# Optimization experiments

Hardware: AMD Instinct MI355X
Metric: run time of the kernel (lower is better)

The kernel has to match this reference:

```python
import jax, jax.numpy as jnp
import numpy as np

SIGMA = 1.0
DELTA = 1.0
TOPK = 10
TOPK_HALF = int(np.around(TOPK / 2))  # 5
EPS = 1e-12


def _cdist(a, b):
    # Euclidean distance matrix, grad-safe sqrt at zero (matches torch.cdist values).
    d2 = (jnp.sum(a * a, axis=1)[:, None]
          + jnp.sum(b * b, axis=1)[None, :]
          - 2.0 * (a @ b.T))
    d2 = jnp.maximum(d2, 0.0)
    pos = d2 > 0.0
    return jnp.where(pos, jnp.sqrt(jnp.where(pos, d2, 1.0)), 0.0)


def _consistency_weights(t_emb):
    # Everything here is under torch.no_grad() in the original.
    N = t_emb.shape[0]
    T_dist = _cdist(t_emb, t_emb)
    W_P = jnp.exp(-(T_dist ** 2) / SIGMA)
    _, idx = jax.lax.top_k(W_P, TOPK)                      # [N, TOPK]
    rows = jnp.arange(N)[:, None]
    W_NN = jnp.zeros_like(W_P).at[rows, idx].set(1.0)      # scatter_ ones
    V = (((W_NN + W_NN.T) / 2) == 1.0).astype(W_P.dtype)   # mutual kNN (symmetric)
    # Vectorized form of the per-row python loop:
    #   W_C_tilda[i, j] = V[i, j] * (sum_k V[i, k] * V[j, k]) / sum_k V[i, k]
    deg = jnp.sum(V, axis=1)                               # >= 1 (self is always a NN)
    overlap = V @ V.T                                      # [N, N] neighbor overlap
    W_C_tilda = V * overlap / deg[:, None]
    topk_half_index = idx[:, :TOPK_HALF]                   # [N, TOPK_HALF]
    W_C_hat = jnp.mean(W_C_tilda[topk_half_index], axis=1) # gather rows, mean -> [N, N]
    W_C = (W_C_hat + W_C_hat.T) / 2
    return (W_P + W_C) / 2


def reference(s_emb, t_emb):
    # disable_mu = 0 -> s_emb NOT normalized; t_emb always normalized.
    t_norm = t_emb / jnp.maximum(
        jnp.linalg.norm(t_emb, axis=1, keepdims=True), EPS)
    N = s_emb.shape[0]
    S_dist = _cdist(s_emb, s_emb)
    S_dist = S_dist / jnp.mean(S_dist, axis=1, keepdims=True)
    W = jax.lax.stop_gradient(_consistency_weights(t_norm))
    off_diag = 1.0 - jnp.eye(N, dtype=W.dtype)
    pos_weight = W * off_diag
    neg_weight = (1.0 - W) * off_diag
    pull = jnp.maximum(S_dist, 0.0) ** 2 * pos_weight
    push = jnp.maximum(DELTA - S_dist, 0.0) ** 2 * neg_weight
    return (jnp.sum(pull) + jnp.sum(push)) / (N * (N - 1))


def setup_inputs() -> dict:
    key = jax.random.key(0)
    k1, k2 = jax.random.split(key)
    N, D = 2048, 1024
    return {
        "s_emb": jax.random.normal(k1, (N, D), dtype=jnp.float32),
        "t_emb": jax.random.normal(k2, (N, D), dtype=jnp.float32),
    }
```

## Files before the change

kernel.cpp:

```cpp
#include <hip/hip_runtime.h>
#include <math.h>

#define N_ 2048
#define D_ 1024
#define TOPK 10
#define TOPK_HALF 5
#define INV_NORM (1.0f / ((float)N_ * (float)(N_ - 1)))

typedef __attribute__((ext_vector_type(8))) short short8;
typedef __attribute__((ext_vector_type(4))) float floatx4;

__device__ __forceinline__ short f2bf(float f) {
  unsigned u = __float_as_uint(f);
  unsigned r = (u + 0x7fffu + ((u >> 16) & 1u)) >> 16;
  return (short)r;
}
__device__ __forceinline__ float bf2f(short b) {
  return __uint_as_float(((unsigned)(unsigned short)b) << 16);
}

__device__ __forceinline__ void gld_lds16(const short* g, short* l) {
  __builtin_amdgcn_global_load_lds(
      (const __attribute__((address_space(1))) unsigned int*)(g),
      (__attribute__((address_space(3))) unsigned int*)(l), 16, 0, 0);
}

__global__ __launch_bounds__(256) void prep_kernel(const float* __restrict__ t,
                                                   const float* __restrict__ s,
                                                   short* __restrict__ tb,
                                                   short* __restrict__ sb,
                                                   float* __restrict__ tt,
                                                   float* __restrict__ ss,
                                                   float* __restrict__ rowsum,
                                                   float* __restrict__ out) {
  int b = blockIdx.x, tid = threadIdx.x;
  __shared__ float red[256];
  if (b == 0) {
    for (int j = tid; j < N_; j += 256) rowsum[j] = 0.f;
    if (tid == 0) out[0] = 0.f;
  }
  if (b < N_) {
    const float* rp = t + (size_t)b * D_;
    short* op = tb + (size_t)b * D_;
    float acc = 0.f;
    for (int k = tid; k < D_; k += 256) { float v = rp[k]; acc += v * v; }
    red[tid] = acc; __syncthreads();
    for (int st = 128; st > 0; st >>= 1) { if (tid < st) red[tid] += red[tid + st]; __syncthreads(); }
    float denom = fmaxf(sqrtf(red[0]), 1e-12f);
    __syncthreads();
    float s2 = 0.f;
    for (int k = tid; k < D_; k += 256) { float v = rp[k] / denom; op[k] = f2bf(v); s2 += v * v; }
    red[tid] = s2; __syncthreads();
    for (int st = 128; st > 0; st >>= 1) { if (tid < st) red[tid] += red[tid + st]; __syncthreads(); }
    if (tid == 0) tt[b] = red[0];
  } else {
    int row = b - N_;
    const float* rp = s + (size_t)row * D_;
    short* op = sb + (size_t)row * D_;
    float acc = 0.f;
    for (int k = tid; k < D_; k += 256) { float v = rp[k]; op[k] = f2bf(v); acc += v * v; }
    red[tid] = acc; __syncthreads();
    for (int st = 128; st > 0; st >>= 1) { if (tid < st) red[tid] += red[tid + st]; __syncthreads(); }
    if (tid == 0) ss[row] = red[0];
  }
}

__global__ __launch_bounds__(256) void gram_mfma_kernel(
    const short* __restrict__ Tb, const short* __restrict__ Sb,
    const float* __restrict__ tt, const float* __restrict__ ss,
    short* __restrict__ WPb, short* __restrict__ Sob,
    float* __restrict__ rowsum) {
  const int mode = blockIdx.z;
  const short* A = mode ? Sb : Tb;
  const float* rn = mode ? ss : tt;
  short* outb = mode ? Sob : WPb;

  __shared__ __align__(16) short As[128 * 64];
  __shared__ __align__(16) short Bs[128 * 64];

  int tid = threadIdx.x;
  int w = tid >> 6, lane = tid & 63;
  int i0 = blockIdx.y * 128, j0 = blockIdx.x * 128;
  int wr = w >> 1, wc = w & 1;
  int quad = lane >> 4, l16 = lane & 15;

  floatx4 acc[4][4] = {};

  int srow = w * 32 + (lane >> 3);
  int scol = (lane & 7) * 8;
  const short* Ag = A + (size_t)(i0 + srow) * D_ + scol;
  const short* Bg = A + (size_t)(j0 + srow) * D_ + scol;
  short* Al = As + srow * 64 + scol;
  short* Bl = Bs + srow * 64 + scol;

  for (int k0 = 0; k0 < D_; k0 += 64) {
    __syncthreads();
#pragma unroll
    for (int q = 0; q < 4; q++) {
      gld_lds16(Ag + k0 + (size_t)q * 8 * D_, Al + q * 8 * 64);
      gld_lds16(Bg + k0 + (size_t)q * 8 * D_, Bl + q * 8 * 64);
    }
    __syncthreads();
#pragma unroll
    for (int ks = 0; ks < 64; ks += 32) {
      short8 af[4], bfr[4];
#pragma unroll
      for (int mt = 0; mt < 4; mt++)
        af[mt] = *(const short8*)&As[(wr * 64 + mt * 16 + l16) * 64 + ks + quad * 8];
#pragma unroll
      for (int nt = 0; nt < 4; nt++)
        bfr[nt] = *(const short8*)&Bs[(wc * 64 + nt * 16 + l16) * 64 + ks + quad * 8];
#pragma unroll
      for (int mt = 0; mt < 4; mt++)
#pragma unroll
        for (int nt = 0; nt < 4; nt++)
          acc[mt][nt] = __builtin_amdgcn_mfma_f32_16x16x32_bf16(af[mt], bfr[nt], acc[mt][nt], 0, 0, 0);
    }
  }

#pragma unroll
  for (int mt = 0; mt < 4; mt++) {
#pragma unroll
    for (int r = 0; r < 4; r++) {
      int i = i0 + wr * 64 + mt * 16 + quad * 4 + r;
      float ri = rn[i];
      float rs = 0.f;
#pragma unroll
      for (int nt = 0; nt < 4; nt++) {
        int j = j0 + wc * 64 + nt * 16 + l16;
        float d2 = fmaxf(ri + rn[j] - 2.f * acc[mt][nt][r], 0.f);
        float o = mode ? sqrtf(d2) : expf(-d2);
        if (i == j) o = mode ? 0.f : 1.f;
        outb[(size_t)i * N_ + j] = f2bf(o);
        rs += o;
      }
      if (mode) {
        rs += __shfl_xor(rs, 1); rs += __shfl_xor(rs, 2);
        rs += __shfl_xor(rs, 4); rs += __shfl_xor(rs, 8);
        if (l16 == 0) atomicAdd(&rowsum[i], rs);
      }
    }
  }
}

__global__ __launch_bounds__(256) void topk_loss_kernel(const short* __restrict__ WPb,
                                                        const short* __restrict__ Sb,
                                                        const float* __restrict__ rowsum,
                                                        int* __restrict__ idx,
                                                        float* __restrict__ out) {
  int row = blockIdx.x, tid = threadIdx.x;
  short8 wp8 = ((const short8*)(WPb + (size_t)row * N_))[tid];
  short8 s8 = ((const short8*)(Sb + (size_t)row * N_))[tid];
  float w[8];
  float rminv = (float)N_ / rowsum[row];
  float local = 0.f;
#pragma unroll
  for (int c = 0; c < 8; c++) {
    w[c] = bf2f(wp8[c]);
    float sv = bf2f(s8[c]) * rminv;
    float d = fmaxf(1.0f - sv, 0.f);
    local += d * d + 0.5f * w[c] * (sv * sv - d * d);
  }
  __shared__ float red[256];
  __shared__ float wv[4];
  __shared__ int wi[4];
  red[tid] = local; __syncthreads();
  for (int st = 128; st > 0; st >>= 1) { if (tid < st) red[tid] += red[tid + st]; __syncthreads(); }
  if (tid == 0) atomicAdd(out, (red[0] - 0.5f) * INV_NORM);

  for (int t = 0; t < TOPK; t++) {
    float bv = -2.f; int bi = 0;
#pragma unroll
    for (int c = 0; c < 8; c++)
      if (w[c] > bv) { bv = w[c]; bi = tid * 8 + c; }
#pragma unroll
    for (int off = 32; off > 0; off >>= 1) {
      float ov = __shfl_down(bv, off);
      int oi = __shfl_down(bi, off);
      if (ov > bv || (ov == bv && oi < bi)) { bv = ov; bi = oi; }
    }
    __syncthreads();
    if ((tid & 63) == 0) { wv[tid >> 6] = bv; wi[tid >> 6] = bi; }
    __syncthreads();
    float b0 = wv[0]; int j0w = wi[0];
#pragma unroll
    for (int u = 1; u < 4; u++)
      if (wv[u] > b0 || (wv[u] == b0 && wi[u] < j0w)) { b0 = wv[u]; j0w = wi[u]; }
    if (tid == 0) idx[row * TOPK + t] = j0w;
    if ((j0w >> 3) == tid) w[j0w & 7] = -1.f;
  }
}

__global__ void mutual_kernel(const int* __restrict__ idx, int* __restrict__ nbr,
                              int* __restrict__ deg) {
  int i = blockIdx.x * blockDim.x + threadIdx.x;
  if (i >= N_) return;
  int cnt = 0;
  for (int k = 0; k < TOPK; k++) {
    int j = idx[i * TOPK + k];
    bool mut = false;
    for (int l = 0; l < TOPK; l++)
      if (idx[j * TOPK + l] == i) mut = true;
    if (mut) nbr[i * TOPK + cnt++] = j;
  }
  deg[i] = cnt;
}

__global__ __launch_bounds__(256) void sparse_wc_kernel(
    const int* __restrict__ idx, const int* __restrict__ nbr,
    const int* __restrict__ deg, const short* __restrict__ Sb,
    const float* __restrict__ rowsum, float* __restrict__ out) {
  int t = blockIdx.x * 256 + threadIdx.x;
  int i = t / (TOPK_HALF * TOPK);
  int r = t % (TOPK_HALF * TOPK);
  int mi = r / TOPK, k = r % TOPK;
  float contrib = 0.f;
  if (i < N_) {
    int m = idx[i * TOPK + mi];
    int dm = deg[m];
    if (k < dm) {
      int col = nbr[m * TOPK + k];
      if (col != i) {
        int dj = deg[col];
        int c = 0;
        for (int a = 0; a < dm; a++) {
          int na = nbr[m * TOPK + a];
          for (int b = 0; b < dj; b++) c += (nbr[col * TOPK + b] == na);
        }
        float v = (float)c / (float)dm * 0.1f;
        float s1 = bf2f(Sb[(size_t)i * N_ + col]) * ((float)N_ / rowsum[i]);
        float d1 = fmaxf(1.f - s1, 0.f);
        float s2 = bf2f(Sb[(size_t)col * N_ + i]) * ((float)N_ / rowsum[col]);
        float d2 = fmaxf(1.f - s2, 0.f);
        contrib = 0.5f * v * ((s1 * s1 - d1 * d1) + (s2 * s2 - d2 * d2));
      }
    }
  }
  __shared__ float red[256];
  red[threadIdx.x] = contrib; __syncthreads();
  for (int st = 128; st > 0; st >>= 1) {
    if (threadIdx.x < st) red[threadIdx.x] += red[threadIdx.x + st];
    __syncthreads();
  }
  if (threadIdx.x == 0) atomicAdd(out, red[0] * INV_NORM);
}

#define SPARSE_BLOCKS ((N_ * TOPK_HALF * TOPK) / 256)

extern "C" void kernel_launch(void* const* d_in, const int* in_sizes, int n_in,
                              void* d_out, int out_size, void* d_ws, size_t ws_size,
                              hipStream_t stream) {
  const float* s_emb = (const float*)d_in[0];
  const float* t_emb = (const float*)d_in[1];
  float* out = (float*)d_out;

  const size_t NN = (size_t)N_ * N_;
  const size_t ND = (size_t)N_ * D_;
  short* t_bf = (short*)d_ws;
  short* s_bf = t_bf + ND;
  short* WPb = s_bf + ND;
  short* Sb = WPb + NN;
  float* tt = (float*)(Sb + NN);
  float* ss = tt + N_;
  float* rowsum = ss + N_;
  int* idx = (int*)(rowsum + N_);
  int* nbr = idx + (size_t)N_ * TOPK;
  int* deg = nbr + (size_t)N_ * TOPK;

  prep_kernel<<<2 * N_, 256, 0, stream>>>(t_emb, s_emb, t_bf, s_bf, tt, ss, rowsum, out);

  dim3 g(N_ / 128, N_ / 128, 2);
  gram_mfma_kernel<<<g, 256, 0, stream>>>(t_bf, s_bf, tt, ss, WPb, Sb, rowsum);

  topk_loss_kernel<<<N_, 256, 0, stream>>>(WPb, Sb, rowsum, idx, out);
  mutual_kernel<<<N_ / 256, 256, 0, stream>>>(idx, nbr, deg);
  sparse_wc_kernel<<<SPARSE_BLOCKS, 256, 0, stream>>>(idx, nbr, deg, Sb, rowsum, out);
}
```

Measured before the change: 172.0 us.

## Double-buffer and swizzle GEMM LDS tiles; use single-wave topk and bitmask mutual kNN

```diff
diff --git a/kernel.cpp b/kernel.cpp
--- a/kernel.cpp
+++ b/kernel.cpp
@@ -24,6 +24,10 @@
       (const __attribute__((address_space(1))) unsigned int*)(g),
       (__attribute__((address_space(3))) unsigned int*)(l), 16, 0, 0);
 }
+
+#define BAR() asm volatile("s_barrier" ::: "memory")
+#define WAIT8_BAR() asm volatile("s_waitcnt vmcnt(8)\ns_barrier" ::: "memory")
+#define WAIT0_BAR() asm volatile("s_waitcnt vmcnt(0)\ns_barrier" ::: "memory")
 
 __global__ __launch_bounds__(256) void prep_kernel(const float* __restrict__ t,
                                                    const float* __restrict__ s,
@@ -75,8 +79,8 @@
   const float* rn = mode ? ss : tt;
   short* outb = mode ? Sob : WPb;
 
-  __shared__ __align__(16) short As[128 * 64];
-  __shared__ __align__(16) short Bs[128 * 64];
+  __shared__ __align__(16) short As[2][128 * 64];
+  __shared__ __align__(16) short Bs[2][128 * 64];
 
   int tid = threadIdx.x;
   int w = tid >> 6, lane = tid & 63;
@@ -87,29 +91,46 @@
   floatx4 acc[4][4] = {};
 
   int srow = w * 32 + (lane >> 3);
-  int scol = (lane & 7) * 8;
-  const short* Ag = A + (size_t)(i0 + srow) * D_ + scol;
-  const short* Bg = A + (size_t)(j0 + srow) * D_ + scol;
-  short* Al = As + srow * 64 + scol;
-  short* Bl = Bs + srow * 64 + scol;
-
-  for (int k0 = 0; k0 < D_; k0 += 64) {
-    __syncthreads();
-#pragma unroll
-    for (int q = 0; q < 4; q++) {
-      gld_lds16(Ag + k0 + (size_t)q * 8 * D_, Al + q * 8 * 64);
-      gld_lds16(Bg + k0 + (size_t)q * 8 * D_, Bl + q * 8 * 64);
-    }
-    __syncthreads();
+  int gchunk = ((lane & 7) ^ (lane >> 3)) * 8;
+  const short* Ag = A + (size_t)(i0 + srow) * D_ + gchunk;
+  const short* Bg = A + (size_t)(j0 + srow) * D_ + gchunk;
+  int sloc = srow * 64 + (lane & 7) * 8;
+
+#define STAGE(buf, k0)                                        \
+  do {                                                        \
+    _Pragma("unroll") for (int q = 0; q < 4; q++) {           \
+      gld_lds16(Ag + (k0) + (size_t)q * 8 * D_, &As[buf][sloc + q * 8 * 64]); \
+      gld_lds16(Bg + (k0) + (size_t)q * 8 * D_, &Bs[buf][sloc + q * 8 * 64]); \
+    }                                                         \
+  } while (0)
+
+  STAGE(0, 0);
+#pragma unroll 2
+  for (int it = 0; it < 16; it++) {
+    int cur = it & 1;
+    if (it) BAR();
+    if (it < 15) {
+      STAGE(!cur, (it + 1) * 64);
+      WAIT8_BAR();
+    } else {
+      WAIT0_BAR();
+    }
+    const short* Ab = As[cur];
+    const short* Bb = Bs[cur];
 #pragma unroll
     for (int ks = 0; ks < 64; ks += 32) {
+      int cb = ks >> 3;
       short8 af[4], bfr[4];
 #pragma unroll
-      for (int mt = 0; mt < 4; mt++)
-        af[mt] = *(const short8*)&As[(wr * 64 + mt * 16 + l16) * 64 + ks + quad * 8];
-#pragma unroll
-      for (int nt = 0; nt < 4; nt++)
-        bfr[nt] = *(const short8*)&Bs[(wc * 64 + nt * 16 + l16) * 64 + ks + quad * 8];
+      for (int mt = 0; mt < 4; mt++) {
+        int r = wr * 64 + mt * 16 + l16;
+        af[mt] = *(const short8*)&Ab[r * 64 + (((cb + quad) ^ (l16 & 7)) << 3)];
+      }
+#pragma unroll
+      for (int nt = 0; nt < 4; nt++) {
+        int r = wc * 64 + nt * 16 + l16;
+        bfr[nt] = *(const short8*)&Bb[r * 64 + (((cb + quad) ^ (l16 & 7)) << 3)];
+      }
 #pragma unroll
       for (int mt = 0; mt < 4; mt++)
 #pragma unroll
@@ -143,89 +164,105 @@
   }
 }
 
-__global__ __launch_bounds__(256) void topk_loss_kernel(const short* __restrict__ WPb,
-                                                        const short* __restrict__ Sb,
-                                                        const float* __restrict__ rowsum,
-                                                        int* __restrict__ idx,
-                                                        float* __restrict__ out) {
-  int row = blockIdx.x, tid = threadIdx.x;
-  short8 wp8 = ((const short8*)(WPb + (size_t)row * N_))[tid];
-  short8 s8 = ((const short8*)(Sb + (size_t)row * N_))[tid];
-  float w[8];
+__global__ __launch_bounds__(64) void topk_loss_kernel(const short* __restrict__ WPb,
+                                                       const short* __restrict__ Sb,
+                                                       const float* __restrict__ rowsum,
+                                                       int* __restrict__ idx,
+                                                       unsigned* __restrict__ mask,
+                                                       float* __restrict__ out) {
+  int row = blockIdx.x, lane = threadIdx.x;
+  const short8* wpr = (const short8*)(WPb + (size_t)row * N_);
+  const short8* sr = (const short8*)(Sb + (size_t)row * N_);
   float rminv = (float)N_ / rowsum[row];
+  float w[32];
   float local = 0.f;
 #pragma unroll
-  for (int c = 0; c < 8; c++) {
-    w[c] = bf2f(wp8[c]);
-    float sv = bf2f(s8[c]) * rminv;
-    float d = fmaxf(1.0f - sv, 0.f);
-    local += d * d + 0.5f * w[c] * (sv * sv - d * d);
-  }
-  __shared__ float red[256];
-  __shared__ float wv[4];
-  __shared__ int wi[4];
-  red[tid] = local; __syncthreads();
-  for (int st = 128; st > 0; st >>= 1) { if (tid < st) red[tid] += red[tid + st]; __syncthreads(); }
-  if (tid == 0) atomicAdd(out, (red[0] - 0.5f) * INV_NORM);
-
+  for (int c4 = 0; c4 < 4; c4++) {
+    short8 wp8 = wpr[lane * 4 + c4];
+    short8 s8 = sr[lane * 4 + c4];
+#pragma unroll
+    for (int e = 0; e < 8; e++) {
+      float wv = bf2f(wp8[e]);
+      w[c4 * 8 + e] = wv;
+      float sv = bf2f(s8[e]) * rminv;
+      float d = fmaxf(1.f - sv, 0.f);
+      local += d * d + 0.5f * wv * (sv * sv - d * d);
+    }
+  }
+#pragma unroll
+  for (int off = 32; off > 0; off >>= 1) local += __shfl_down(local, off);
+  if (lane == 0) {
+    atomicAdd(out, (local - 0.5f) * INV_NORM);
+    mask[row] = 0u;
+  }
+  int base = lane * 32;
+  int sel[TOPK];
   for (int t = 0; t < TOPK; t++) {
     float bv = -2.f; int bi = 0;
 #pragma unroll
-    for (int c = 0; c < 8; c++)
-      if (w[c] > bv) { bv = w[c]; bi = tid * 8 + c; }
+    for (int c = 0; c < 32; c++)
+      if (w[c] > bv) { bv = w[c]; bi = base + c; }
 #pragma unroll
     for (int off = 32; off > 0; off >>= 1) {
       float ov = __shfl_down(bv, off);
       int oi = __shfl_down(bi, off);
       if (ov > bv || (ov == bv && oi < bi)) { bv = ov; bi = oi; }
     }
-    __syncthreads();
-    if ((tid & 63) == 0) { wv[tid >> 6] = bv; wi[tid >> 6] = bi; }
-    __syncthreads();
-    float b0 = wv[0]; int j0w = wi[0];
-#pragma unroll
-    for (int u = 1; u < 4; u++)
-      if (wv[u] > b0 || (wv[u] == b0 && wi[u] < j0w)) { b0 = wv[u]; j0w = wi[u]; }
-    if (tid == 0) idx[row * TOPK + t] = j0w;
-    if ((j0w >> 3) == tid) w[j0w & 7] = -1.f;
-  }
-}
-
-__global__ void mutual_kernel(const int* __restrict__ idx, int* __restrict__ nbr,
-                              int* __restrict__ deg) {
-  int i = blockIdx.x * blockDim.x + threadIdx.x;
-  if (i >= N_) return;
-  int cnt = 0;
-  for (int k = 0; k < TOPK; k++) {
-    int j = idx[i * TOPK + k];
-    bool mut = false;
-    for (int l = 0; l < TOPK; l++)
-      if (idx[j * TOPK + l] == i) mut = true;
-    if (mut) nbr[i * TOPK + cnt++] = j;
-  }
-  deg[i] = cnt;
+    bi = __shfl(bi, 0);
+    sel[t] = bi;
+    bool mine = (bi >> 5) == lane;
+    int cc = bi & 31;
+#pragma unroll
+    for (int c = 0; c < 32; c++)
+      if (mine && cc == c) w[c] = -1.f;
+  }
+  if (lane == 0) {
+#pragma unroll
+    for (int t = 0; t < TOPK; t++) idx[row * TOPK + t] = sel[t];
+  }
+}
+
+__global__ __launch_bounds__(256) void mutual_kernel(const int* __restrict__ idx,
+                                                     unsigned* __restrict__ mask) {
+  int t = blockIdx.x * 256 + threadIdx.x;
+  int i = t >> 4, k = t & 15;
+  if (i >= N_ || k >= TOPK) return;
+  int j = idx[i * TOPK + k];
+  bool mut = false;
+#pragma unroll
+  for (int l = 0; l < TOPK; l++) mut |= (idx[j * TOPK + l] == i);
+  if (mut) atomicOr(&mask[i], 1u << k);
 }
 
 __global__ __launch_bounds__(256) void sparse_wc_kernel(
-    const int* __restrict__ idx, const int* __restrict__ nbr,
-    const int* __restrict__ deg, const short* __restrict__ Sb,
-    const float* __restrict__ rowsum, float* __restrict__ out) {
+    const int* __restrict__ idx, const unsigned* __restrict__ mask,
+    const short* __restrict__ Sb, const float* __restrict__ rowsum,
+    float* __restrict__ out) {
   int t = blockIdx.x * 256 + threadIdx.x;
-  int i = t / (TOPK_HALF * TOPK);
-  int r = t % (TOPK_HALF * TOPK);
-  int mi = r / TOPK, k = r % TOPK;
+  int i = t >> 6, r = t & 63;
   float contrib = 0.f;
-  if (i < N_) {
+  if (i < N_ && r < TOPK_HALF * TOPK) {
+    int mi = r / TOPK, k = r - mi * TOPK;
     int m = idx[i * TOPK + mi];
-    int dm = deg[m];
-    if (k < dm) {
-      int col = nbr[m * TOPK + k];
+    unsigned mm = mask[m];
+    if ((mm >> k) & 1u) {
+      int col = idx[m * TOPK + k];
       if (col != i) {
-        int dj = deg[col];
+        int dm = __popc(mm);
+        unsigned mc = mask[col];
+        int jm[TOPK], jc[TOPK];
+#pragma unroll
+        for (int l = 0; l < TOPK; l++) jm[l] = idx[m * TOPK + l];
+#pragma unroll
+        for (int l = 0; l < TOPK; l++) jc[l] = idx[col * TOPK + l];
         int c = 0;
-        for (int a = 0; a < dm; a++) {
-          int na = nbr[m * TOPK + a];
-          for (int b = 0; b < dj; b++) c += (nbr[col * TOPK + b] == na);
+#pragma unroll
+        for (int a = 0; a < TOPK; a++) {
+          if ((mm >> a) & 1u) {
+            int na = jm[a];
+#pragma unroll
+            for (int b = 0; b < TOPK; b++) c += (((mc >> b) & 1u) && (jc[b] == na));
+          }
         }
         float v = (float)c / (float)dm * 0.1f;
         float s1 = bf2f(Sb[(size_t)i * N_ + col]) * ((float)N_ / rowsum[i]);
@@ -244,8 +281,6 @@
   }
   if (threadIdx.x == 0) atomicAdd(out, red[0] * INV_NORM);
 }
-
-#define SPARSE_BLOCKS ((N_ * TOPK_HALF * TOPK) / 256)
 
 extern "C" void kernel_launch(void* const* d_in, const int* in_sizes, int n_in,
                               void* d_out, int out_size, void* d_ws, size_t ws_size,
@@ -264,15 +299,14 @@
   float* ss = tt + N_;
   float* rowsum = ss + N_;
   int* idx = (int*)(rowsum + N_);
-  int* nbr = idx + (size_t)N_ * TOPK;
-  int* deg = nbr + (size_t)N_ * TOPK;
+  unsigned* mask = (unsigned*)(idx + (size_t)N_ * TOPK);
 
   prep_kernel<<<2 * N_, 256, 0, stream>>>(t_emb, s_emb, t_bf, s_bf, tt, ss, rowsum, out);
 
   dim3 g(N_ / 128, N_ / 128, 2);
   gram_mfma_kernel<<<g, 256, 0, stream>>>(t_bf, s_bf, tt, ss, WPb, Sb, rowsum);
 
-  topk_loss_kernel<<<N_, 256, 0, stream>>>(WPb, Sb, rowsum, idx, out);
-  mutual_kernel<<<N_ / 256, 256, 0, stream>>>(idx, nbr, deg);
-  sparse_wc_kernel<<<SPARSE_BLOCKS, 256, 0, stream>>>(idx, nbr, deg, Sb, rowsum, out);
-}
+  topk_loss_kernel<<<N_, 64, 0, stream>>>(WPb, Sb, rowsum, idx, mask, out);
+  mutual_kernel<<<N_ * 16 / 256, 256, 0, stream>>>(idx, mask);
+  sparse_wc_kernel<<<N_ * 64 / 256, 256, 0, stream>>>(idx, mask, Sb, rowsum, out);
+}
```

Measured after the change: 149.7 us. 12.9% less time.
